# Kernel optimization log

Measured on AMD Instinct MI355X. Metric: run time of the kernel, lower is better.

The kernel has to match this reference:

```python
import jax, jax.numpy as jnp
import numpy as np

E, D, H, K, T = 16, 1024, 2048, 2, 2048


def setup_inputs() -> dict:
    key = jax.random.key(0)
    k = jax.random.split(key, 7)
    scale = 0.02
    return {
        "inp": jax.random.normal(k[0], (T, D), dtype=jnp.float32),
        "gate_idx": jax.random.randint(k[1], (T, K), 0, E, dtype=jnp.int64),
        "gate_score": jax.random.uniform(k[2], (T, K), dtype=jnp.float32),
        "w1": jax.random.normal(k[3], (E, H, D), dtype=jnp.float32) * scale,
        "b1": jnp.zeros((E, H), dtype=jnp.float32),
        "w2": jax.random.normal(k[4], (E, D, H), dtype=jnp.float32) * scale,
        "b2": jnp.zeros((E, D), dtype=jnp.float32),
    }


def reference(inp, gate_idx, gate_score, w1, b1, w2, b2):
    num_expert = w1.shape[0]
    top_k = gate_idx.shape[1]
    d_model = inp.shape[1]
    # expand each token top_k times (repeat_interleave along dim 0)
    x = jnp.repeat(inp, top_k, axis=0)           # [T*K, D]
    g = gate_idx.reshape(-1)                      # [T*K]
    o = jnp.zeros((x.shape[0], d_model), dtype=x.dtype)
    # static loop over experts; output masked by expert assignment (same math
    # as the per-expert gather/scatter in the original)
    for i in range(num_expert):
        h = jax.nn.gelu(x @ w1[i].T + b1[i])      # [T*K, H]
        y = h @ w2[i].T + b2[i]                   # [T*K, D]
        o = o + jnp.where((g == i)[:, None], y, jnp.zeros((), x.dtype))
    # combine top_k expert outputs with gate scores (bmm in the original)
    out = jnp.einsum("nk,nkd->nd", gate_score, o.reshape(-1, top_k, d_model))
    return out
```

## Files before the change

### kernel.cpp

```cpp
#include <hip/hip_runtime.h>
#include <hip/hip_bf16.h>
#include <stdint.h>


#define E_ 16
#define D_ 1024
#define H_ 2048
#define K_ 2
#define T_ 2048
#define NP_ (T_ * K_)
#define MTS_ 48

using short8 = __attribute__((ext_vector_type(8))) short;
using f32x4  = __attribute__((ext_vector_type(4))) float;

__device__ __forceinline__ unsigned short f2bf(float f) {
  union { float f; unsigned u; } x; x.f = f;
  unsigned r = x.u + 0x7fffu + ((x.u >> 16) & 1u);
  return (unsigned short)(r >> 16);
}

__device__ __forceinline__ float gelu_f(float x) {
  float u = 1.5957691216057308f * (x + 0.044715f * x * x * x);
  return x / (1.f + __expf(-u));
}

__device__ __forceinline__ void waitv8() {
  asm volatile("s_waitcnt vmcnt(8)" ::: "memory");
  __builtin_amdgcn_sched_barrier(0);
}
__device__ __forceinline__ void waitv0() {
  asm volatile("s_waitcnt vmcnt(0)" ::: "memory");
  __builtin_amdgcn_sched_barrier(0);
}
__device__ __forceinline__ void barrier_only() {
  __builtin_amdgcn_sched_barrier(0);
  __builtin_amdgcn_s_barrier();
  __builtin_amdgcn_sched_barrier(0);
}
__device__ __forceinline__ void lgkm0_barrier() {
  asm volatile("s_waitcnt lgkmcnt(0)" ::: "memory");
  __builtin_amdgcn_sched_barrier(0);
  __builtin_amdgcn_s_barrier();
  __builtin_amdgcn_sched_barrier(0);
}

__global__ void prep_kernel(const float* __restrict__ inp,
                            unsigned short* __restrict__ xb,
                            const int* __restrict__ gidx,
                            int* __restrict__ rows,
                            int* __restrict__ offsets,
                            int2* __restrict__ tiles) {
  if (blockIdx.x == 0) {
    __shared__ int cnt[E_], cur[E_];
    int tid = threadIdx.x;
    if (tid < E_) cnt[tid] = 0;
    __syncthreads();
    for (int p = tid; p < NP_; p += 256) atomicAdd(&cnt[gidx[p]], 1);
    __syncthreads();
    if (tid == 0) {
      int acc = 0;
      for (int e = 0; e < E_; ++e) { offsets[e] = acc; cur[e] = acc; acc += cnt[e]; }
      offsets[E_] = acc;
      int k = 0;
      for (int e = 0; e < E_; ++e)
        for (int m = offsets[e]; m < offsets[e] + cnt[e]; m += 128)
          tiles[k++] = make_int2(e, m);
      for (; k < MTS_; ++k) tiles[k] = make_int2(-1, 0);
    }
    __syncthreads();
    for (int p = tid; p < NP_; p += 256) {
      int e = gidx[p];
      int pos = atomicAdd(&cur[e], 1);
      rows[pos] = p;
    }
  } else {
    const int n4 = T_ * D_ / 4;
    const int stride = (gridDim.x - 1) * blockDim.x;
    for (int i = (blockIdx.x - 1) * blockDim.x + threadIdx.x; i < n4; i += stride) {
      float4 v = reinterpret_cast<const float4*>(inp)[i];
      ushort4 o = make_ushort4(f2bf(v.x), f2bf(v.y), f2bf(v.z), f2bf(v.w));
      reinterpret_cast<ushort4*>(xb)[i] = o;
    }
  }
}

#define GLOAD16(g, l)                                                        \
  __builtin_amdgcn_global_load_lds(                                          \
      (const __attribute__((address_space(1))) unsigned int*)(const void*)(g), \
      (__attribute__((address_space(3))) unsigned int*)(void*)(l), 16, 0, 0)

template<bool IS1>
__global__ __launch_bounds__(256, 3)
void moe_gemm(const unsigned short* __restrict__ A0,
              const float* __restrict__ W,
              const float* __restrict__ bias,
              const int* __restrict__ rows,
              const int* __restrict__ offsets,
              const int2* __restrict__ tiles,
              const float* __restrict__ score,
              unsigned short* __restrict__ Hout,
              float* __restrict__ Yout)
{
  constexpr int BM = 128, BN = 64, BK = 64;
  constexpr int KD = IS1 ? D_ : H_;
  constexpr int NN = IS1 ? H_ : D_;
  constexpr int NT = KD / BK;

  const int2 tile = tiles[blockIdx.y];
  const int e = tile.x;
  if (e < 0) return;
  const int s0   = tile.y;
  const int send = offsets[e + 1];
  const int n0   = blockIdx.x * BN;

  __shared__ unsigned short As[2][BM][BK];
  __shared__ unsigned short Bs[2][BN][BK];
  __shared__ int rowsrc[BM];
  __shared__ int rowdst[BM];

  const int tid  = threadIdx.x;
  const int lane = tid & 63;
  const int wid  = tid >> 6;

  if (tid < BM) {
    int s = s0 + tid;
    bool v = s < send;
    int sc2 = v ? s : s0;
    if (IS1) {
      rowsrc[tid] = rows[sc2] >> 1;
      rowdst[tid] = v ? s : -1;
    } else {
      rowsrc[tid] = sc2;
      rowdst[tid] = v ? rows[s] : -1;
    }
  }
  __syncthreads();

  const int arow  = lane >> 3;
  const int aslot = (lane & 7) ^ arow;
  const unsigned short* gA[4];
#pragma unroll
  for (int i = 0; i < 4; ++i)
    gA[i] = A0 + (size_t)rowsrc[wid * 32 + i * 8 + arow] * KD + aslot * 8;

  const int brow = tid >> 3, boct = tid & 7;
  const float* gB0 = W + (size_t)e * NN * KD + (size_t)(n0 + brow) * KD + boct * 4;
  const float* gB2 = gB0 + (size_t)32 * KD;

  const int wr = wid >> 1, wc = wid & 1;
  const int fr = lane & 15, fh = lane >> 4;

  f32x4 acc[4][2] = {};
  float4 breg0[4], breg1[4];

  auto issueA = [&](int buf, int kk) {
#pragma unroll
    for (int i = 0; i < 4; ++i)
      GLOAD16(gA[i] + kk, &As[buf][wid * 32 + i * 8][0]);
  };
  auto issueB = [&](float4* br, int kk) {
    br[0] = *reinterpret_cast<const float4*>(gB0 + kk);
    br[1] = *reinterpret_cast<const float4*>(gB0 + kk + 32);
    br[2] = *reinterpret_cast<const float4*>(gB2 + kk);
    br[3] = *reinterpret_cast<const float4*>(gB2 + kk + 32);
  };
  auto writeB = [&](int buf, const float4* br) {
#pragma unroll
    for (int p = 0; p < 4; ++p) {
      int row = (p & 2) ? brow + 32 : brow;
      int kl0 = boct * 4 + ((p & 1) ? 32 : 0);
      ushort4 u;
      const float* f = &br[p].x;
      u.x = f2bf(f[0]); u.y = f2bf(f[1]); u.z = f2bf(f[2]); u.w = f2bf(f[3]);
      int idx = (((kl0 >> 3) ^ (row & 7)) << 3) + (kl0 & 7);
      *reinterpret_cast<ushort4*>(&Bs[buf][row][idx]) = u;
    }
  };
  auto compute = [&](int buf) {
    short8 af[4][2], bv[2][2];
#pragma unroll
    for (int mi = 0; mi < 4; ++mi) {
      const int row = wr * 64 + mi * 16 + fr;
#pragma unroll
      for (int ks = 0; ks < 2; ++ks) {
        const int slot = (ks * 4 + fh) ^ (row & 7);
        af[mi][ks] = *reinterpret_cast<const short8*>(&As[buf][row][slot * 8]);
      }
    }
#pragma unroll
    for (int ni = 0; ni < 2; ++ni) {
      const int row = wc * 32 + ni * 16 + fr;
#pragma unroll
      for (int ks = 0; ks < 2; ++ks) {
        const int slot = (ks * 4 + fh) ^ (row & 7);
        bv[ni][ks] = *reinterpret_cast<const short8*>(&Bs[buf][row][slot * 8]);
      }
    }
#pragma unroll
    for (int ks = 0; ks < 2; ++ks)
#pragma unroll
      for (int mi = 0; mi < 4; ++mi)
#pragma unroll
        for (int ni = 0; ni < 2; ++ni)
          acc[mi][ni] = __builtin_amdgcn_mfma_f32_16x16x32_bf16(
              af[mi][ks], bv[ni][ks], acc[mi][ni], 0, 0, 0);
  };

  issueA(0, 0);       issueB(breg0, 0);
  issueA(1, BK);      issueB(breg1, BK);
  waitv8();
  writeB(0, breg0);
  lgkm0_barrier();

  for (int t = 0; t < NT; t += 2) {
    compute(0);
    barrier_only();
    if (t + 2 < NT) {
      issueA(0, (t + 2) * BK); issueB(breg0, (t + 2) * BK);
      waitv8();
    } else {
      waitv0();
    }
    writeB(1, breg1);
    lgkm0_barrier();
    compute(1);
    barrier_only();
    if (t + 2 < NT) {
      if (t + 3 < NT) { issueA(1, (t + 3) * BK); issueB(breg1, (t + 3) * BK); waitv8(); }
      else            { waitv0(); }
      writeB(0, breg0);
      lgkm0_barrier();
    }
  }

  const float* biasE = bias + (size_t)e * NN + n0;
#pragma unroll
  for (int mi = 0; mi < 4; ++mi) {
#pragma unroll
    for (int j = 0; j < 4; ++j) {
      int rt  = wr * 64 + mi * 16 + fh * 4 + j;
      int dst = rowdst[rt];
      if (dst < 0) continue;
      float sc = IS1 ? 0.f : score[dst];
#pragma unroll
      for (int ni = 0; ni < 2; ++ni) {
        int col = wc * 32 + ni * 16 + fr;
        float v = acc[mi][ni][j] + biasE[col];
        if (IS1) {
          Hout[(size_t)dst * H_ + n0 + col] = f2bf(gelu_f(v));
        } else {
          Yout[(size_t)dst * D_ + n0 + col] = v * sc;
        }
      }
    }
  }
}

__global__ void combine_kernel(const float* __restrict__ y,
                               float* __restrict__ out) {
  const int DQ = D_ / 4;
  int i = blockIdx.x * blockDim.x + threadIdx.x;
  int t = i / DQ, d = i % DQ;
  const float4* y4 = reinterpret_cast<const float4*>(y);
  float4 a = y4[(size_t)(2 * t) * DQ + d];
  float4 b = y4[(size_t)(2 * t + 1) * DQ + d];
  reinterpret_cast<float4*>(out)[i] =
      make_float4(a.x + b.x, a.y + b.y, a.z + b.z, a.w + b.w);
}

extern "C" void kernel_launch(void* const* d_in, const int* in_sizes, int n_in,
                              void* d_out, int out_size, void* d_ws, size_t ws_size,
                              hipStream_t stream) {
  const float* inp    = (const float*)d_in[0];
  const int*   gidx   = (const int*)d_in[1];
  const float* gscore = (const float*)d_in[2];
  const float* w1     = (const float*)d_in[3];
  const float* b1     = (const float*)d_in[4];
  const float* w2     = (const float*)d_in[5];
  const float* b2     = (const float*)d_in[6];
  float* out = (float*)d_out;

  char* ws = (char*)d_ws;
  size_t o = 0;
  auto alloc = [&](size_t bytes) {
    void* p = ws + o;
    o = (o + bytes + 255) & ~(size_t)255;
    return p;
  };
  unsigned short* xb   = (unsigned short*)alloc((size_t)T_ * D_ * 2);
  unsigned short* hbuf = (unsigned short*)alloc((size_t)NP_ * H_ * 2);
  float*          ybuf = (float*)alloc((size_t)NP_ * D_ * 4);
  int*            rows = (int*)alloc(NP_ * 4);
  int*         offsets = (int*)alloc((E_ + 1) * 4);
  int2*          tiles = (int2*)alloc(MTS_ * 8);

  prep_kernel<<<dim3(513), dim3(256), 0, stream>>>(inp, xb, gidx, rows,
                                                   offsets, tiles);

  moe_gemm<true><<<dim3(H_ / 64, MTS_), dim3(256), 0, stream>>>(
      xb, w1, b1, rows, offsets, tiles, gscore, hbuf, (float*)nullptr);
  moe_gemm<false><<<dim3(D_ / 64, MTS_), dim3(256), 0, stream>>>(
      hbuf, w2, b2, rows, offsets, tiles, gscore, (unsigned short*)nullptr, ybuf);

  combine_kernel<<<dim3(T_ * D_ / 4 / 256), dim3(256), 0, stream>>>(ybuf, out);
}
```

Measured before the change: 142.4 us.

## Widen MoE GEMM N tile to 128 with 4x4 MFMA per warp

Doubles the GEMM block tile in N from 64 to 128. Each warp now computes a 64x64 output sub-tile with a 4x4 grid of MFMA accumulators, and the B-tile staging loads 8 float4 per thread. The goal is more reuse of each A tile and a higher MFMA-to-load ratio, with half as many blocks launched along N. In exchange, register pressure rises, launch bounds drop from 3 to 2 blocks per CU, the vmcnt wait threshold is adjusted to 12, and fewer blocks may leave CUs underfilled.

```diff
diff --git a/kernel.cpp b/kernel.cpp
--- a/kernel.cpp
+++ b/kernel.cpp
@@ -25,8 +25,8 @@
   return x / (1.f + __expf(-u));
 }
 
-__device__ __forceinline__ void waitv8() {
-  asm volatile("s_waitcnt vmcnt(8)" ::: "memory");
+__device__ __forceinline__ void waitv12() {
+  asm volatile("s_waitcnt vmcnt(12)" ::: "memory");
   __builtin_amdgcn_sched_barrier(0);
 }
 __device__ __forceinline__ void waitv0() {
@@ -91,7 +91,7 @@
       (__attribute__((address_space(3))) unsigned int*)(void*)(l), 16, 0, 0)
 
 template<bool IS1>
-__global__ __launch_bounds__(256, 3)
+__global__ __launch_bounds__(256, 2)
 void moe_gemm(const unsigned short* __restrict__ A0,
               const float* __restrict__ W,
               const float* __restrict__ bias,
@@ -102,7 +102,7 @@
               unsigned short* __restrict__ Hout,
               float* __restrict__ Yout)
 {
-  constexpr int BM = 128, BN = 64, BK = 64;
+  constexpr int BM = 128, BN = 128, BK = 64;
   constexpr int KD = IS1 ? D_ : H_;
   constexpr int NN = IS1 ? H_ : D_;
   constexpr int NT = KD / BK;
@@ -146,13 +146,12 @@
 
   const int brow = tid >> 3, boct = tid & 7;
   const float* gB0 = W + (size_t)e * NN * KD + (size_t)(n0 + brow) * KD + boct * 4;
-  const float* gB2 = gB0 + (size_t)32 * KD;
 
   const int wr = wid >> 1, wc = wid & 1;
   const int fr = lane & 15, fh = lane >> 4;
 
-  f32x4 acc[4][2] = {};
-  float4 breg0[4], breg1[4];
+  f32x4 acc[4][4] = {};
+  float4 breg0[8], breg1[8];
 
   auto issueA = [&](int buf, int kk) {
 #pragma unroll
@@ -160,56 +159,57 @@
       GLOAD16(gA[i] + kk, &As[buf][wid * 32 + i * 8][0]);
   };
   auto issueB = [&](float4* br, int kk) {
-    br[0] = *reinterpret_cast<const float4*>(gB0 + kk);
-    br[1] = *reinterpret_cast<const float4*>(gB0 + kk + 32);
-    br[2] = *reinterpret_cast<const float4*>(gB2 + kk);
-    br[3] = *reinterpret_cast<const float4*>(gB2 + kk + 32);
+#pragma unroll
+    for (int p = 0; p < 4; ++p) {
+#pragma unroll
+      for (int h = 0; h < 2; ++h)
+        br[p * 2 + h] = *reinterpret_cast<const float4*>(
+            gB0 + (size_t)p * 32 * KD + kk + h * 32);
+    }
   };
   auto writeB = [&](int buf, const float4* br) {
 #pragma unroll
     for (int p = 0; p < 4; ++p) {
-      int row = (p & 2) ? brow + 32 : brow;
-      int kl0 = boct * 4 + ((p & 1) ? 32 : 0);
-      ushort4 u;
-      const float* f = &br[p].x;
-      u.x = f2bf(f[0]); u.y = f2bf(f[1]); u.z = f2bf(f[2]); u.w = f2bf(f[3]);
-      int idx = (((kl0 >> 3) ^ (row & 7)) << 3) + (kl0 & 7);
-      *reinterpret_cast<ushort4*>(&Bs[buf][row][idx]) = u;
+#pragma unroll
+      for (int h = 0; h < 2; ++h) {
+        int row = brow + p * 32;
+        int kl0 = boct * 4 + h * 32;
+        ushort4 u;
+        const float* f = &br[p * 2 + h].x;
+        u.x = f2bf(f[0]); u.y = f2bf(f[1]); u.z = f2bf(f[2]); u.w = f2bf(f[3]);
+        int idx = (((kl0 >> 3) ^ (row & 7)) << 3) + (kl0 & 7);
+        *reinterpret_cast<ushort4*>(&Bs[buf][row][idx]) = u;
+      }
     }
   };
   auto compute = [&](int buf) {
-    short8 af[4][2], bv[2][2];
-#pragma unroll
-    for (int mi = 0; mi < 4; ++mi) {
-      const int row = wr * 64 + mi * 16 + fr;
-#pragma unroll
-      for (int ks = 0; ks < 2; ++ks) {
+#pragma unroll
+    for (int ks = 0; ks < 2; ++ks) {
+      short8 af[4], bv[4];
+#pragma unroll
+      for (int mi = 0; mi < 4; ++mi) {
+        const int row = wr * 64 + mi * 16 + fr;
         const int slot = (ks * 4 + fh) ^ (row & 7);
-        af[mi][ks] = *reinterpret_cast<const short8*>(&As[buf][row][slot * 8]);
+        af[mi] = *reinterpret_cast<const short8*>(&As[buf][row][slot * 8]);
       }
-    }
-#pragma unroll
-    for (int ni = 0; ni < 2; ++ni) {
-      const int row = wc * 32 + ni * 16 + fr;
-#pragma unroll
-      for (int ks = 0; ks < 2; ++ks) {
+#pragma unroll
+      for (int ni = 0; ni < 4; ++ni) {
+        const int row = wc * 64 + ni * 16 + fr;
         const int slot = (ks * 4 + fh) ^ (row & 7);
-        bv[ni][ks] = *reinterpret_cast<const short8*>(&Bs[buf][row][slot * 8]);
+        bv[ni] = *reinterpret_cast<const short8*>(&Bs[buf][row][slot * 8]);
       }
-    }
-#pragma unroll
-    for (int ks = 0; ks < 2; ++ks)
 #pragma unroll
       for (int mi = 0; mi < 4; ++mi)
 #pragma unroll
-        for (int ni = 0; ni < 2; ++ni)
+        for (int ni = 0; ni < 4; ++ni)
           acc[mi][ni] = __builtin_amdgcn_mfma_f32_16x16x32_bf16(
-              af[mi][ks], bv[ni][ks], acc[mi][ni], 0, 0, 0);
+              af[mi], bv[ni], acc[mi][ni], 0, 0, 0);
+    }
   };
 
   issueA(0, 0);       issueB(breg0, 0);
   issueA(1, BK);      issueB(breg1, BK);
-  waitv8();
+  waitv12();
   writeB(0, breg0);
   lgkm0_barrier();
 
@@ -218,7 +218,7 @@
     barrier_only();
     if (t + 2 < NT) {
       issueA(0, (t + 2) * BK); issueB(breg0, (t + 2) * BK);
-      waitv8();
+      waitv12();
     } else {
       waitv0();
     }
@@ -227,7 +227,7 @@
     compute(1);
     barrier_only();
     if (t + 2 < NT) {
-      if (t + 3 < NT) { issueA(1, (t + 3) * BK); issueB(breg1, (t + 3) * BK); waitv8(); }
+      if (t + 3 < NT) { issueA(1, (t + 3) * BK); issueB(breg1, (t + 3) * BK); waitv12(); }
       else            { waitv0(); }
       writeB(0, breg0);
       lgkm0_barrier();
@@ -244,8 +244,8 @@
       if (dst < 0) continue;
       float sc = IS1 ? 0.f : score[dst];
 #pragma unroll
-      for (int ni = 0; ni < 2; ++ni) {
-        int col = wc * 32 + ni * 16 + fr;
+      for (int ni = 0; ni < 4; ++ni) {
+        int col = wc * 64 + ni * 16 + fr;
         float v = acc[mi][ni][j] + biasE[col];
         if (IS1) {
           Hout[(size_t)dst * H_ + n0 + col] = f2bf(gelu_f(v));
@@ -298,9 +298,9 @@
   prep_kernel<<<dim3(513), dim3(256), 0, stream>>>(inp, xb, gidx, rows,
                                                    offsets, tiles);
 
-  moe_gemm<true><<<dim3(H_ / 64, MTS_), dim3(256), 0, stream>>>(
+  moe_gemm<true><<<dim3(H_ / 128, MTS_), dim3(256), 0, stream>>>(
       xb, w1, b1, rows, offsets, tiles, gscore, hbuf, (float*)nullptr);
-  moe_gemm<false><<<dim3(D_ / 64, MTS_), dim3(256), 0, stream>>>(
+  moe_gemm<false><<<dim3(D_ / 128, MTS_), dim3(256), 0, stream>>>(
       hbuf, w2, b2, rows, offsets, tiles, gscore, (unsigned short*)nullptr, ybuf);
 
   combine_kernel<<<dim3(T_ * D_ / 4 / 256), dim3(256), 0, stream>>>(ybuf, out);
```

Result: slower. 156.6 us (+10.0%).
